# Kernel tuning notes

Measured on AMD Instinct MI355X. Metric: run time of the kernel, lower is better.

## Reference

```python
import math
import jax, jax.numpy as jnp
import numpy as np

N = 100000
E_RAND = 800000
IN_F, HID, OUT_F, HEADS = 128, 64, 64, 4
NOISE_SCALE = 1.0 * math.sqrt(2.0 * math.log(1.25 / 0.05))  # dp_rate=1, eps=1, del=0.05


def setup_inputs() -> dict:
    key = jax.random.key(0)
    ks = jax.random.split(key, 12)
    x = jax.random.normal(ks[0], (N, IN_F), dtype=jnp.float32)
    src_r = jax.random.randint(ks[1], (E_RAND,), 0, N, dtype=jnp.int32)
    dst_r = jax.random.randint(ks[2], (E_RAND,), 0, N, dtype=jnp.int32)
    loops = jnp.arange(N, dtype=jnp.int32)  # add_self_loop
    src = jnp.concatenate([src_r, loops])
    dst = jnp.concatenate([dst_r, loops])
    # layer 0: GATConv(in=128, out=64, heads=4)
    s0 = 1.0 / math.sqrt(IN_F)
    W0 = jax.random.normal(ks[3], (IN_F, HEADS * HID), dtype=jnp.float32) * s0
    al0 = jax.random.normal(ks[4], (HEADS, HID), dtype=jnp.float32) * 0.1
    ar0 = jax.random.normal(ks[5], (HEADS, HID), dtype=jnp.float32) * 0.1
    b0 = jnp.zeros((HEADS * HID,), dtype=jnp.float32)
    # layer 1: GATConv(in=256, out=64, heads=1)
    s1 = 1.0 / math.sqrt(HEADS * HID)
    W1 = jax.random.normal(ks[6], (HEADS * HID, OUT_F), dtype=jnp.float32) * s1
    al1 = jax.random.normal(ks[7], (1, OUT_F), dtype=jnp.float32) * 0.1
    ar1 = jax.random.normal(ks[8], (1, OUT_F), dtype=jnp.float32) * 0.1
    b1 = jnp.zeros((OUT_F,), dtype=jnp.float32)
    # DP gaussian noise added after first GAT layer (torch.normal(0,1,x.shape))
    noise = jax.random.normal(ks[9], (N, HEADS * HID), dtype=jnp.float32)
    return {"x": x, "src": src, "dst": dst, "W0": W0, "al0": al0, "ar0": ar0,
            "b0": b0, "W1": W1, "al1": al1, "ar1": ar1, "b1": b1, "noise": noise}


def gat_conv(x, src, dst, W, al, ar, b, apply_act):
    """DGL GATConv: per-edge attention, edge softmax over dst, scatter-sum."""
    H, D = al.shape
    h = (x @ W).reshape(-1, H, D)                      # [N,H,D]
    el = jnp.sum(h * al, axis=-1)                      # [N,H]
    er = jnp.sum(h * ar, axis=-1)                      # [N,H]
    e = jax.nn.leaky_relu(el[src] + er[dst], 0.2)      # [E,H]
    emax = jax.ops.segment_max(e, dst, num_segments=N) # [N,H]
    a = jnp.exp(e - emax[dst])
    denom = jax.ops.segment_sum(a, dst, num_segments=N)
    alpha = a / denom[dst]                             # [E,H] edge softmax
    msg = h[src] * alpha[:, :, None]                   # [E,H,D]
    out = jax.ops.segment_sum(msg, dst, num_segments=N) + b.reshape(1, H, D)
    if apply_act:
        out = jax.nn.leaky_relu(out, 0.01)             # F.leaky_relu default slope
    return out.reshape(-1, H * D)                      # flatten(1)


def reference(x, src, dst, W0, al0, ar0, b0, W1, al1, ar1, b1, noise):
    h = gat_conv(x, src, dst, W0, al0, ar0, b0, apply_act=True)   # [N, 256]
    h = h + NOISE_SCALE * noise                                   # DP noise after layer 0
    out = gat_conv(h, src, dst, W1, al1, ar1, b1, apply_act=False)  # [N, 64]
    return out
```

## Files before the change

kernel.cpp:

```cpp
#include <hip/hip_runtime.h>
#include <hip/hip_bf16.h>
#include <math.h>

#define IN_F 128
#define HID 64
#define HEADS 4
#define HD0 (HEADS * HID)
#define OUT_F 64
#define NOISE_SCALE 2.5372725354060904f

typedef __bf16 bf16x8 __attribute__((ext_vector_type(8)));
typedef float f32x4 __attribute__((ext_vector_type(4)));
typedef float f4 __attribute__((ext_vector_type(4)));
typedef unsigned int u4 __attribute__((ext_vector_type(4)));

__device__ __forceinline__ float bf2f(unsigned short u) {
    return __uint_as_float(((unsigned)u) << 16);
}
__device__ __forceinline__ unsigned short f2bf(float f) {
    unsigned u = __float_as_uint(f);
    u = u + 0x7fffu + ((u >> 16) & 1u);
    return (unsigned short)(u >> 16);
}

__device__ __forceinline__ void acc8(float* acc, const uint4& u, float wt) {
    acc[0] += wt * __uint_as_float(u.x << 16);
    acc[1] += wt * __uint_as_float(u.x & 0xffff0000u);
    acc[2] += wt * __uint_as_float(u.y << 16);
    acc[3] += wt * __uint_as_float(u.y & 0xffff0000u);
    acc[4] += wt * __uint_as_float(u.z << 16);
    acc[5] += wt * __uint_as_float(u.z & 0xffff0000u);
    acc[6] += wt * __uint_as_float(u.w << 16);
    acc[7] += wt * __uint_as_float(u.w & 0xffff0000u);
}

__device__ __forceinline__ uint4 pack8(const float4& a, const float4& b) {
    uint4 r;
    r.x = (unsigned)f2bf(a.x) | ((unsigned)f2bf(a.y) << 16);
    r.y = (unsigned)f2bf(a.z) | ((unsigned)f2bf(a.w) << 16);
    r.z = (unsigned)f2bf(b.x) | ((unsigned)f2bf(b.y) << 16);
    r.w = (unsigned)f2bf(b.z) | ((unsigned)f2bf(b.w) << 16);
    return r;
}

__global__ __launch_bounds__(256) void prep_kernel(
    int* __restrict__ deg, int N,
    unsigned long long* __restrict__ combo, int ntiles,
    const float* __restrict__ W0, unsigned short* __restrict__ W0t,
    const float* __restrict__ W1, unsigned short* __restrict__ W1t) {
    const int b = blockIdx.x;
    int i = b * 256 + threadIdx.x;
    if (i < N) deg[i] = 0;
    if (i < ntiles) combo[i] = 0ULL;
    if (b < (IN_F * HD0) / 256) {
        int n = i / IN_F, k = i % IN_F;
        W0t[i] = f2bf(W0[(size_t)k * HD0 + n]);
    } else if (b < (IN_F * HD0) / 256 + (HD0 * OUT_F) / 256) {
        int j = i - IN_F * HD0;
        int n = j / HD0, k = j % HD0;
        W1t[j] = f2bf(W1[(size_t)k * OUT_F + n]);
    }
}

template <int K, int H, int NT, bool CVT>
__global__ __launch_bounds__(256) void gemm_fused_kernel(
    const void* __restrict__ Asrc, const unsigned short* __restrict__ Bt,
    unsigned short* __restrict__ C, const float* __restrict__ al,
    const float* __restrict__ ar, float* __restrict__ el,
    float* __restrict__ er, int M, int NC) {
    constexpr int BSTR = K + 8;
    constexpr int ASTR = 40;
    constexpr int NROWS = 64 * NT;
    constexpr int CSTR = NROWS + 8;
    __shared__ __align__(16) unsigned short Bs[NROWS * BSTR];
    __shared__ __align__(16) unsigned short As[128 * ASTR];
    const unsigned short* Ab = (const unsigned short*)Asrc;
    const float* Af = (const float*)Asrc;
    const int tid = threadIdx.x;
    const int lane = tid & 63, w = tid >> 6;
    const int row0 = blockIdx.y * 128;
    const int n0 = blockIdx.x * NROWS;
    for (int i = tid; i < NROWS * (K / 8); i += 256) {
        int n = i / (K / 8), kc = i % (K / 8);
        *(uint4*)(Bs + n * BSTR + kc * 8) =
            *(const uint4*)(Bt + (size_t)(n0 + n) * K + kc * 8);
    }
    f32x4 acc[2][4 * NT] = {};
    const int q = lane >> 4, c = lane & 15;
    const int r_st = tid >> 1, hh = tid & 1;
    for (int k0 = 0; k0 < K; k0 += 32) {
        int gr = row0 + r_st;
        uint4 av0 = make_uint4(0, 0, 0, 0), av1 = make_uint4(0, 0, 0, 0);
        if (gr < M) {
            if (CVT) {
                const float* xp = Af + (size_t)gr * K + k0 + hh * 16;
                const float4 fa = *(const float4*)xp;
                const float4 fb = *(const float4*)(xp + 4);
                const float4 fc = *(const float4*)(xp + 8);
                const float4 fd = *(const float4*)(xp + 12);
                av0 = pack8(fa, fb);
                av1 = pack8(fc, fd);
            } else {
                const unsigned short* ap = Ab + (size_t)gr * K + k0 + hh * 16;
                av0 = *(const uint4*)(ap);
                av1 = *(const uint4*)(ap + 8);
            }
        }
        __syncthreads();
        *(uint4*)(As + r_st * ASTR + hh * 16) = av0;
        *(uint4*)(As + r_st * ASTR + hh * 16 + 8) = av1;
        __syncthreads();
        bf16x8 af[2], bfr[4 * NT];
        af[0] = *(const bf16x8*)(As + (w * 32 + c) * ASTR + q * 8);
        af[1] = *(const bf16x8*)(As + (w * 32 + 16 + c) * ASTR + q * 8);
#pragma unroll
        for (int nt = 0; nt < 4 * NT; ++nt)
            bfr[nt] = *(const bf16x8*)(Bs + (nt * 16 + c) * BSTR + k0 + q * 8);
#pragma unroll
        for (int mt = 0; mt < 2; ++mt)
#pragma unroll
            for (int nt = 0; nt < 4 * NT; ++nt)
                acc[mt][nt] = __builtin_amdgcn_mfma_f32_16x16x32_bf16(
                    af[mt], bfr[nt], acc[mt][nt], 0, 0, 0);
    }
    float alv[4 * NT], arv[4 * NT];
#pragma unroll
    for (int nt = 0; nt < 4 * NT; ++nt) {
        alv[nt] = al[n0 + nt * 16 + c];
        arv[nt] = ar[n0 + nt * 16 + c];
    }
    __syncthreads();
    unsigned short* Cs = Bs;
    const int headbase = n0 >> 6;
#pragma unroll
    for (int mt = 0; mt < 2; ++mt) {
#pragma unroll
        for (int r = 0; r < 4; ++r) {
            const int row = w * 32 + mt * 16 + q * 4 + r;
            const int grow = row0 + row;
            const bool ok = grow < M;
#pragma unroll
            for (int g = 0; g < NT; ++g) {
                float elp = 0.f, erp = 0.f;
#pragma unroll
                for (int t = 0; t < 4; ++t) {
                    int nt = g * 4 + t;
                    float v = acc[mt][nt][r];
                    elp += v * alv[nt];
                    erp += v * arv[nt];
                    Cs[row * CSTR + nt * 16 + c] = f2bf(v);
                }
#pragma unroll
                for (int o = 8; o > 0; o >>= 1) {
                    elp += __shfl_down(elp, o, 16);
                    erp += __shfl_down(erp, o, 16);
                }
                if (c == 0 && ok) {
                    el[(size_t)grow * H + headbase + g] = elp;
                    er[(size_t)grow * H + headbase + g] = erp;
                }
            }
        }
    }
    __syncthreads();
    constexpr int CPR = NROWS / 8;
    for (int i = tid; i < 128 * CPR; i += 256) {
        int row = i / CPR, ch = i % CPR;
        int grow = row0 + row;
        if (grow < M)
            *(uint4*)(C + (size_t)grow * NC + n0 + ch * 8) =
                *(const uint4*)(Cs + row * CSTR + ch * 8);
    }
}

__global__ __launch_bounds__(256) void degree_kernel(
    const int* __restrict__ dst, int* __restrict__ deg, int E) {
    int e = blockIdx.x * 256 + threadIdx.x;
    if (e < E) atomicAdd(&deg[dst[e]], 1);
}

__global__ __launch_bounds__(256) void scan_fused_kernel(
    const int* __restrict__ deg, int* __restrict__ off, int* __restrict__ cur,
    unsigned long long* __restrict__ combo, int N, int E) {
    const int t = blockIdx.x;
    __shared__ int s[256];
    __shared__ int sbase;
    const int tid = threadIdx.x;
    const int i = t * 256 + tid;
    const int v = (i < N) ? deg[i] : 0;
    s[tid] = v;
    __syncthreads();
    for (int d = 1; d < 256; d <<= 1) {
        int tt = (tid >= d) ? s[tid - d] : 0;
        __syncthreads();
        s[tid] += tt;
        __syncthreads();
    }
    const int tilesum = s[255];
    if (tid == 0) {
        if (t == 0) {
            atomicExch(&combo[0], (2ULL << 32) | (unsigned)tilesum);
            sbase = 0;
        } else {
            atomicExch(&combo[t], (1ULL << 32) | (unsigned)tilesum);
            int run = 0;
            int j = t - 1;
            while (true) {
                unsigned long long c;
                do {
                    c = atomicAdd(&combo[j], 0ULL);
                } while ((c >> 32) == 0ULL);
                run += (int)(c & 0xffffffffULL);
                if ((c >> 32) == 2ULL) break;
                --j;
            }
            sbase = run;
            atomicExch(&combo[t], (2ULL << 32) | (unsigned)(run + tilesum));
        }
    }
    __syncthreads();
    const int base = sbase;
    if (i < N) {
        int o = base + s[tid] - v;
        off[i] = o;
        cur[i] = o;
    }
    if (i == 0) off[N] = E;
}

__global__ __launch_bounds__(256) void fill_csr_kernel(
    const int* __restrict__ src, const int* __restrict__ dst,
    int* __restrict__ cur, int* __restrict__ csr_src, int E) {
    int e = blockIdx.x * 256 + threadIdx.x;
    if (e >= E) return;
    int d = dst[e];
    int pos = atomicAdd(&cur[d], 1);
    csr_src[pos] = src[e];
}

__global__ __launch_bounds__(256) void agg0_kernel(
    const int* __restrict__ off, const int* __restrict__ csr_src,
    const unsigned short* __restrict__ h,
    const float* __restrict__ el,
    const float* __restrict__ er,
    const float* __restrict__ b0, const float* __restrict__ noise,
    unsigned short* __restrict__ out, int N) {
    int gt = blockIdx.x * 256 + threadIdx.x;
    int n = gt >> 5;
    if (n >= N) return;
    const int lane = gt & 31;
    const int hd = lane >> 3;
    const int f0 = lane << 3;
    const float ern = er[(size_t)n * 4 + hd];
    const int beg = off[n];
    const int last = off[n + 1] - 1;
    float acc[8] = {0.f, 0.f, 0.f, 0.f, 0.f, 0.f, 0.f, 0.f};
    float l = 0.f;
    for (int p = beg; p <= last; p += 4) {
        int i1 = p + 1, i2 = p + 2, i3 = p + 3;
        const bool v1 = i1 <= last, v2 = i2 <= last, v3 = i3 <= last;
        i1 = v1 ? i1 : last;
        i2 = v2 ? i2 : last;
        i3 = v3 ? i3 : last;
        const int s0 = csr_src[p],  s1 = csr_src[i1];
        const int s2 = csr_src[i2], s3 = csr_src[i3];
        float e0 = el[(size_t)s0 * 4 + hd] + ern;
        float e1 = el[(size_t)s1 * 4 + hd] + ern;
        float e2 = el[(size_t)s2 * 4 + hd] + ern;
        float e3 = el[(size_t)s3 * 4 + hd] + ern;
        const uint4 u0 = *(const uint4*)(h + (size_t)s0 * HD0 + f0);
        const uint4 u1 = *(const uint4*)(h + (size_t)s1 * HD0 + f0);
        const uint4 u2 = *(const uint4*)(h + (size_t)s2 * HD0 + f0);
        const uint4 u3 = *(const uint4*)(h + (size_t)s3 * HD0 + f0);
        e0 = e0 > 0.f ? e0 : 0.2f * e0;
        e1 = e1 > 0.f ? e1 : 0.2f * e1;
        e2 = e2 > 0.f ? e2 : 0.2f * e2;
        e3 = e3 > 0.f ? e3 : 0.2f * e3;
        const float w0 = __expf(e0);
        const float w1 = v1 ? __expf(e1) : 0.f;
        const float w2 = v2 ? __expf(e2) : 0.f;
        const float w3 = v3 ? __expf(e3) : 0.f;
        acc8(acc, u0, w0);
        acc8(acc, u1, w1);
        acc8(acc, u2, w2);
        acc8(acc, u3, w3);
        l += (w0 + w1) + (w2 + w3);
    }
    const float rd = 1.f / l;
    const float4 ba = *(const float4*)(b0 + f0);
    const float4 bb = *(const float4*)(b0 + f0 + 4);
    const f4 na = __builtin_nontemporal_load((const f4*)(noise + (size_t)n * HD0 + f0));
    const f4 nb = __builtin_nontemporal_load((const f4*)(noise + (size_t)n * HD0 + f0 + 4));
    float o[8];
    o[0] = acc[0] * rd + ba.x;
    o[1] = acc[1] * rd + ba.y;
    o[2] = acc[2] * rd + ba.z;
    o[3] = acc[3] * rd + ba.w;
    o[4] = acc[4] * rd + bb.x;
    o[5] = acc[5] * rd + bb.y;
    o[6] = acc[6] * rd + bb.z;
    o[7] = acc[7] * rd + bb.w;
#pragma unroll
    for (int j = 0; j < 8; ++j) o[j] = o[j] > 0.f ? o[j] : 0.01f * o[j];
    o[0] += NOISE_SCALE * na.x;
    o[1] += NOISE_SCALE * na.y;
    o[2] += NOISE_SCALE * na.z;
    o[3] += NOISE_SCALE * na.w;
    o[4] += NOISE_SCALE * nb.x;
    o[5] += NOISE_SCALE * nb.y;
    o[6] += NOISE_SCALE * nb.z;
    o[7] += NOISE_SCALE * nb.w;
    uint4 ov;
    ov.x = (unsigned)f2bf(o[0]) | ((unsigned)f2bf(o[1]) << 16);
    ov.y = (unsigned)f2bf(o[2]) | ((unsigned)f2bf(o[3]) << 16);
    ov.z = (unsigned)f2bf(o[4]) | ((unsigned)f2bf(o[5]) << 16);
    ov.w = (unsigned)f2bf(o[6]) | ((unsigned)f2bf(o[7]) << 16);
    *(uint4*)(out + (size_t)n * HD0 + f0) = ov;
}

__global__ __launch_bounds__(256) void agg1_kernel(
    const int* __restrict__ off, const int* __restrict__ csr_src,
    const unsigned short* __restrict__ h,
    const float* __restrict__ el,
    const float* __restrict__ er,
    const float* __restrict__ b1, float* __restrict__ out, int N) {
    int gt = blockIdx.x * 256 + threadIdx.x;
    int n = gt >> 4;
    if (n >= N) return;
    const int lane = gt & 15;
    const int f0 = lane << 2;
    const float ern = er[n];
    const int beg = off[n];
    const int last = off[n + 1] - 1;
    float a0 = 0.f, a1 = 0.f, a2 = 0.f, a3 = 0.f, l = 0.f;
    for (int p = beg; p <= last; p += 4) {
        int i1 = p + 1, i2 = p + 2, i3 = p + 3;
        const bool v1 = i1 <= last, v2 = i2 <= last, v3 = i3 <= last;
        i1 = v1 ? i1 : last;
        i2 = v2 ? i2 : last;
        i3 = v3 ? i3 : last;
        const int s0 = csr_src[p],  s1 = csr_src[i1];
        const int s2 = csr_src[i2], s3 = csr_src[i3];
        float e0 = el[s0] + ern;
        float e1 = el[s1] + ern;
        float e2 = el[s2] + ern;
        float e3 = el[s3] + ern;
        const ushort4 u0 = *(const ushort4*)(h + (size_t)s0 * 64 + f0);
        const ushort4 u1 = *(const ushort4*)(h + (size_t)s1 * 64 + f0);
        const ushort4 u2 = *(const ushort4*)(h + (size_t)s2 * 64 + f0);
        const ushort4 u3 = *(const ushort4*)(h + (size_t)s3 * 64 + f0);
        e0 = e0 > 0.f ? e0 : 0.2f * e0;
        e1 = e1 > 0.f ? e1 : 0.2f * e1;
        e2 = e2 > 0.f ? e2 : 0.2f * e2;
        e3 = e3 > 0.f ? e3 : 0.2f * e3;
        const float w0 = __expf(e0);
        const float w1 = v1 ? __expf(e1) : 0.f;
        const float w2 = v2 ? __expf(e2) : 0.f;
        const float w3 = v3 ? __expf(e3) : 0.f;
        a0 += w0 * bf2f(u0.x) + w1 * bf2f(u1.x) + w2 * bf2f(u2.x) + w3 * bf2f(u3.x);
        a1 += w0 * bf2f(u0.y) + w1 * bf2f(u1.y) + w2 * bf2f(u2.y) + w3 * bf2f(u3.y);
        a2 += w0 * bf2f(u0.z) + w1 * bf2f(u1.z) + w2 * bf2f(u2.z) + w3 * bf2f(u3.z);
        a3 += w0 * bf2f(u0.w) + w1 * bf2f(u1.w) + w2 * bf2f(u2.w) + w3 * bf2f(u3.w);
        l += (w0 + w1) + (w2 + w3);
    }
    const float rd = 1.f / l;
    const float4 bv = *(const float4*)(b1 + f0);
    float4 o;
    o.x = a0 * rd + bv.x;
    o.y = a1 * rd + bv.y;
    o.z = a2 * rd + bv.z;
    o.w = a3 * rd + bv.w;
    *(float4*)(out + (size_t)n * 64 + f0) = o;
}

extern "C" void kernel_launch(void* const* d_in, const int* in_sizes, int n_in,
                              void* d_out, int out_size, void* d_ws, size_t ws_size,
                              hipStream_t stream) {
    const float* x     = (const float*)d_in[0];
    const int*   src   = (const int*)d_in[1];
    const int*   dst   = (const int*)d_in[2];
    const float* W0    = (const float*)d_in[3];
    const float* al0   = (const float*)d_in[4];
    const float* ar0   = (const float*)d_in[5];
    const float* b0    = (const float*)d_in[6];
    const float* W1    = (const float*)d_in[7];
    const float* al1   = (const float*)d_in[8];
    const float* ar1   = (const float*)d_in[9];
    const float* b1    = (const float*)d_in[10];
    const float* noise = (const float*)d_in[11];

    const int N = in_sizes[0] / IN_F;
    const int E = in_sizes[1];
    const int NB = (N + 255) / 256;

    char* p = (char*)d_ws;
    unsigned short* h0     = (unsigned short*)p; p += (size_t)N * HD0 * 2;
    unsigned short* agg0b  = (unsigned short*)p; p += (size_t)N * HD0 * 2;
    unsigned short* h1     = (unsigned short*)p; p += (size_t)N * OUT_F * 2;
    unsigned short* W0t    = (unsigned short*)p; p += (size_t)IN_F * HD0 * 2;
    unsigned short* W1t    = (unsigned short*)p; p += (size_t)HD0 * OUT_F * 2;
    float* el     = (float*)p; p += (size_t)N * HEADS * 4;
    float* er     = (float*)p; p += (size_t)N * HEADS * 4;
    int* deg    = (int*)p; p += (size_t)N * 4;
    int* cur    = (int*)p; p += (size_t)N * 4;
    int* off    = (int*)p; p += ((size_t)N + 4) * 4;
    unsigned long long* combo = (unsigned long long*)p; p += 512 * 8;
    int* csr_src= (int*)p; p += (size_t)E * 4;

    prep_kernel<<<NB, 256, 0, stream>>>(deg, N, combo, NB, W0, W0t, W1, W1t);

    degree_kernel<<<(E + 255) / 256, 256, 0, stream>>>(dst, deg, E);
    scan_fused_kernel<<<NB, 256, 0, stream>>>(deg, off, cur, combo, N, E);
    fill_csr_kernel<<<(E + 255) / 256, 256, 0, stream>>>(src, dst, cur, csr_src, E);

    const int MB = (N + 127) / 128;

    {
        dim3 grid(HD0 / 128, MB);
        gemm_fused_kernel<IN_F, HEADS, 2, true><<<grid, 256, 0, stream>>>(
            (const void*)x, W0t, h0, al0, ar0, el, er, N, HD0);
    }
    agg0_kernel<<<(unsigned)(((size_t)N * 32 + 255) / 256), 256, 0, stream>>>(
        off, csr_src, h0, el, er, b0, noise, agg0b, N);

    {
        dim3 grid(OUT_F / 64, MB);
        gemm_fused_kernel<HD0, 1, 1, false><<<grid, 256, 0, stream>>>(
            (const void*)agg0b, W1t, h1, al1, ar1, el, er, N, OUT_F);
    }
    agg1_kernel<<<(unsigned)(((size_t)N * 16 + 255) / 256), 256, 0, stream>>>(
        off, csr_src, h1, el, er, b1, (float*)d_out, N);
}
```

Measured before the change: 435.3 us.

## Fuse layer-1 GEMM and attention logits into layer-0 aggregation kernel

The layer-0 aggregation now stages each block's 8 output rows in shared memory as bf16 and immediately multiplies them by W1 with MFMA 16x16x32 instructions. The same kernel computes the layer-1 el/er logits through shuffle reductions and writes h1, el1 and er1 directly. This removes the 256-wide intermediate write and read and one kernel launch. In exchange, half of each 16-row MFMA tile is zero padding, a block barrier sits after the irregular gather loop, and W1 is reloaded from global memory by every block.

```diff
diff --git a/kernel.cpp b/kernel.cpp
--- a/kernel.cpp
+++ b/kernel.cpp
@@ -238,84 +238,147 @@
     csr_src[pos] = src[e];
 }
 
-__global__ __launch_bounds__(256) void agg0_kernel(
+__global__ __launch_bounds__(256) void agg0_fused_kernel(
     const int* __restrict__ off, const int* __restrict__ csr_src,
     const unsigned short* __restrict__ h,
     const float* __restrict__ el,
     const float* __restrict__ er,
     const float* __restrict__ b0, const float* __restrict__ noise,
-    unsigned short* __restrict__ out, int N) {
-    int gt = blockIdx.x * 256 + threadIdx.x;
-    int n = gt >> 5;
-    if (n >= N) return;
-    const int lane = gt & 31;
+    const unsigned short* __restrict__ W1t,
+    const float* __restrict__ al1, const float* __restrict__ ar1,
+    unsigned short* __restrict__ h1,
+    float* __restrict__ el1, float* __restrict__ er1, int N) {
+    constexpr int SSTR = 264;
+    __shared__ __align__(16) unsigned short smA[16 * SSTR];
+    __shared__ float elw[4][8], erw[4][8];
+    const int tid = threadIdx.x;
+    const int nd = tid >> 5;
+    const int n = blockIdx.x * 8 + nd;
+    const bool valid = n < N;
+    const int lane = tid & 31;
     const int hd = lane >> 3;
     const int f0 = lane << 3;
-    const float ern = er[(size_t)n * 4 + hd];
-    const int beg = off[n];
-    const int last = off[n + 1] - 1;
+    for (int i = tid; i < 264; i += 256)
+        *(uint4*)(smA + 8 * SSTR + i * 8) = make_uint4(0, 0, 0, 0);
     float acc[8] = {0.f, 0.f, 0.f, 0.f, 0.f, 0.f, 0.f, 0.f};
     float l = 0.f;
-    for (int p = beg; p <= last; p += 4) {
-        int i1 = p + 1, i2 = p + 2, i3 = p + 3;
-        const bool v1 = i1 <= last, v2 = i2 <= last, v3 = i3 <= last;
-        i1 = v1 ? i1 : last;
-        i2 = v2 ? i2 : last;
-        i3 = v3 ? i3 : last;
-        const int s0 = csr_src[p],  s1 = csr_src[i1];
-        const int s2 = csr_src[i2], s3 = csr_src[i3];
-        float e0 = el[(size_t)s0 * 4 + hd] + ern;
-        float e1 = el[(size_t)s1 * 4 + hd] + ern;
-        float e2 = el[(size_t)s2 * 4 + hd] + ern;
-        float e3 = el[(size_t)s3 * 4 + hd] + ern;
-        const uint4 u0 = *(const uint4*)(h + (size_t)s0 * HD0 + f0);
-        const uint4 u1 = *(const uint4*)(h + (size_t)s1 * HD0 + f0);
-        const uint4 u2 = *(const uint4*)(h + (size_t)s2 * HD0 + f0);
-        const uint4 u3 = *(const uint4*)(h + (size_t)s3 * HD0 + f0);
-        e0 = e0 > 0.f ? e0 : 0.2f * e0;
-        e1 = e1 > 0.f ? e1 : 0.2f * e1;
-        e2 = e2 > 0.f ? e2 : 0.2f * e2;
-        e3 = e3 > 0.f ? e3 : 0.2f * e3;
-        const float w0 = __expf(e0);
-        const float w1 = v1 ? __expf(e1) : 0.f;
-        const float w2 = v2 ? __expf(e2) : 0.f;
-        const float w3 = v3 ? __expf(e3) : 0.f;
-        acc8(acc, u0, w0);
-        acc8(acc, u1, w1);
-        acc8(acc, u2, w2);
-        acc8(acc, u3, w3);
-        l += (w0 + w1) + (w2 + w3);
-    }
-    const float rd = 1.f / l;
-    const float4 ba = *(const float4*)(b0 + f0);
-    const float4 bb = *(const float4*)(b0 + f0 + 4);
-    const f4 na = __builtin_nontemporal_load((const f4*)(noise + (size_t)n * HD0 + f0));
-    const f4 nb = __builtin_nontemporal_load((const f4*)(noise + (size_t)n * HD0 + f0 + 4));
-    float o[8];
-    o[0] = acc[0] * rd + ba.x;
-    o[1] = acc[1] * rd + ba.y;
-    o[2] = acc[2] * rd + ba.z;
-    o[3] = acc[3] * rd + ba.w;
-    o[4] = acc[4] * rd + bb.x;
-    o[5] = acc[5] * rd + bb.y;
-    o[6] = acc[6] * rd + bb.z;
-    o[7] = acc[7] * rd + bb.w;
-#pragma unroll
-    for (int j = 0; j < 8; ++j) o[j] = o[j] > 0.f ? o[j] : 0.01f * o[j];
-    o[0] += NOISE_SCALE * na.x;
-    o[1] += NOISE_SCALE * na.y;
-    o[2] += NOISE_SCALE * na.z;
-    o[3] += NOISE_SCALE * na.w;
-    o[4] += NOISE_SCALE * nb.x;
-    o[5] += NOISE_SCALE * nb.y;
-    o[6] += NOISE_SCALE * nb.z;
-    o[7] += NOISE_SCALE * nb.w;
-    uint4 ov;
-    ov.x = (unsigned)f2bf(o[0]) | ((unsigned)f2bf(o[1]) << 16);
-    ov.y = (unsigned)f2bf(o[2]) | ((unsigned)f2bf(o[3]) << 16);
-    ov.z = (unsigned)f2bf(o[4]) | ((unsigned)f2bf(o[5]) << 16);
-    ov.w = (unsigned)f2bf(o[6]) | ((unsigned)f2bf(o[7]) << 16);
-    *(uint4*)(out + (size_t)n * HD0 + f0) = ov;
+    if (valid) {
+        const float ern = er[(size_t)n * 4 + hd];
+        const int beg = off[n];
+        const int last = off[n + 1] - 1;
+        for (int p = beg; p <= last; p += 4) {
+            int i1 = p + 1, i2 = p + 2, i3 = p + 3;
+            const bool v1 = i1 <= last, v2 = i2 <= last, v3 = i3 <= last;
+            i1 = v1 ? i1 : last;
+            i2 = v2 ? i2 : last;
+            i3 = v3 ? i3 : last;
+            const int s0 = csr_src[p],  s1 = csr_src[i1];
+            const int s2 = csr_src[i2], s3 = csr_src[i3];
+            float e0 = el[(size_t)s0 * 4 + hd] + ern;
+            float e1 = el[(size_t)s1 * 4 + hd] + ern;
+            float e2 = el[(size_t)s2 * 4 + hd] + ern;
+            float e3 = el[(size_t)s3 * 4 + hd] + ern;
+            const uint4 u0 = *(const uint4*)(h + (size_t)s0 * HD0 + f0);
+            const uint4 u1 = *(const uint4*)(h + (size_t)s1 * HD0 + f0);
+            const uint4 u2 = *(const uint4*)(h + (size_t)s2 * HD0 + f0);
+            const uint4 u3 = *(const uint4*)(h + (size_t)s3 * HD0 + f0);
+            e0 = e0 > 0.f ? e0 : 0.2f * e0;
+            e1 = e1 > 0.f ? e1 : 0.2f * e1;
+            e2 = e2 > 0.f ? e2 : 0.2f * e2;
+            e3 = e3 > 0.f ? e3 : 0.2f * e3;
+            const float w0 = __expf(e0);
+            const float w1 = v1 ? __expf(e1) : 0.f;
+            const float w2 = v2 ? __expf(e2) : 0.f;
+            const float w3 = v3 ? __expf(e3) : 0.f;
+            acc8(acc, u0, w0);
+            acc8(acc, u1, w1);
+            acc8(acc, u2, w2);
+            acc8(acc, u3, w3);
+            l += (w0 + w1) + (w2 + w3);
+        }
+        const float rd = 1.f / l;
+        const float4 ba = *(const float4*)(b0 + f0);
+        const float4 bb = *(const float4*)(b0 + f0 + 4);
+        const f4 na = __builtin_nontemporal_load((const f4*)(noise + (size_t)n * HD0 + f0));
+        const f4 nb = __builtin_nontemporal_load((const f4*)(noise + (size_t)n * HD0 + f0 + 4));
+        float o[8];
+        o[0] = acc[0] * rd + ba.x;
+        o[1] = acc[1] * rd + ba.y;
+        o[2] = acc[2] * rd + ba.z;
+        o[3] = acc[3] * rd + ba.w;
+        o[4] = acc[4] * rd + bb.x;
+        o[5] = acc[5] * rd + bb.y;
+        o[6] = acc[6] * rd + bb.z;
+        o[7] = acc[7] * rd + bb.w;
+#pragma unroll
+        for (int j = 0; j < 8; ++j) o[j] = o[j] > 0.f ? o[j] : 0.01f * o[j];
+        o[0] += NOISE_SCALE * na.x;
+        o[1] += NOISE_SCALE * na.y;
+        o[2] += NOISE_SCALE * na.z;
+        o[3] += NOISE_SCALE * na.w;
+        o[4] += NOISE_SCALE * nb.x;
+        o[5] += NOISE_SCALE * nb.y;
+        o[6] += NOISE_SCALE * nb.z;
+        o[7] += NOISE_SCALE * nb.w;
+        uint4 ov;
+        ov.x = (unsigned)f2bf(o[0]) | ((unsigned)f2bf(o[1]) << 16);
+        ov.y = (unsigned)f2bf(o[2]) | ((unsigned)f2bf(o[3]) << 16);
+        ov.z = (unsigned)f2bf(o[4]) | ((unsigned)f2bf(o[5]) << 16);
+        ov.w = (unsigned)f2bf(o[6]) | ((unsigned)f2bf(o[7]) << 16);
+        *(uint4*)(smA + nd * SSTR + f0) = ov;
+    } else {
+        *(uint4*)(smA + nd * SSTR + f0) = make_uint4(0, 0, 0, 0);
+    }
+    __syncthreads();
+    const int w = tid >> 6;
+    const int q = (tid >> 4) & 3;
+    const int c = tid & 15;
+    f32x4 a2 = {};
+#pragma unroll
+    for (int k0 = 0; k0 < HD0; k0 += 32) {
+        bf16x8 af = *(const bf16x8*)(smA + c * SSTR + k0 + q * 8);
+        bf16x8 bfr = *(const bf16x8*)(W1t + (size_t)(w * 16 + c) * HD0 + k0 + q * 8);
+        a2 = __builtin_amdgcn_mfma_f32_16x16x32_bf16(af, bfr, a2, 0, 0, 0);
+    }
+    const float alv = al1[w * 16 + c];
+    const float arv = ar1[w * 16 + c];
+    float pel[4], per_[4];
+#pragma unroll
+    for (int r = 0; r < 4; ++r) {
+        pel[r] = a2[r] * alv;
+        per_[r] = a2[r] * arv;
+    }
+#pragma unroll
+    for (int m = 1; m <= 8; m <<= 1) {
+#pragma unroll
+        for (int r = 0; r < 4; ++r) {
+            pel[r] += __shfl_xor(pel[r], m);
+            per_[r] += __shfl_xor(per_[r], m);
+        }
+    }
+    if (c == 0 && q < 2) {
+#pragma unroll
+        for (int r = 0; r < 4; ++r) {
+            elw[w][q * 4 + r] = pel[r];
+            erw[w][q * 4 + r] = per_[r];
+        }
+    }
+    if (q < 2) {
+#pragma unroll
+        for (int r = 0; r < 4; ++r) {
+            int row = q * 4 + r;
+            int g = blockIdx.x * 8 + row;
+            if (g < N) h1[(size_t)g * OUT_F + w * 16 + c] = f2bf(a2[r]);
+        }
+    }
+    __syncthreads();
+    if (tid < 8) {
+        int g = blockIdx.x * 8 + tid;
+        if (g < N) {
+            el1[g] = elw[0][tid] + elw[1][tid] + elw[2][tid] + elw[3][tid];
+            er1[g] = erw[0][tid] + erw[1][tid] + erw[2][tid] + erw[3][tid];
+        }
+    }
 }
 
 __global__ __launch_bounds__(256) void agg1_kernel(
@@ -395,12 +458,13 @@
 
     char* p = (char*)d_ws;
     unsigned short* h0     = (unsigned short*)p; p += (size_t)N * HD0 * 2;
-    unsigned short* agg0b  = (unsigned short*)p; p += (size_t)N * HD0 * 2;
     unsigned short* h1     = (unsigned short*)p; p += (size_t)N * OUT_F * 2;
     unsigned short* W0t    = (unsigned short*)p; p += (size_t)IN_F * HD0 * 2;
     unsigned short* W1t    = (unsigned short*)p; p += (size_t)HD0 * OUT_F * 2;
     float* el     = (float*)p; p += (size_t)N * HEADS * 4;
     float* er     = (float*)p; p += (size_t)N * HEADS * 4;
+    float* el1    = (float*)p; p += (size_t)N * 4;
+    float* er1    = (float*)p; p += (size_t)N * 4;
     int* deg    = (int*)p; p += (size_t)N * 4;
     int* cur    = (int*)p; p += (size_t)N * 4;
     int* off    = (int*)p; p += ((size_t)N + 4) * 4;
@@ -420,14 +484,10 @@
         gemm_fused_kernel<IN_F, HEADS, 2, true><<<grid, 256, 0, stream>>>(
             (const void*)x, W0t, h0, al0, ar0, el, er, N, HD0);
     }
-    agg0_kernel<<<(unsigned)(((size_t)N * 32 + 255) / 256), 256, 0, stream>>>(
-        off, csr_src, h0, el, er, b0, noise, agg0b, N);
-
-    {
-        dim3 grid(OUT_F / 64, MB);
-        gemm_fused_kernel<HD0, 1, 1, false><<<grid, 256, 0, stream>>>(
-            (const void*)agg0b, W1t, h1, al1, ar1, el, er, N, OUT_F);
-    }
+
+    agg0_fused_kernel<<<(N + 7) / 8, 256, 0, stream>>>(
+        off, csr_src, h0, el, er, b0, noise, W1t, al1, ar1, h1, el1, er1, N);
+
     agg1_kernel<<<(unsigned)(((size_t)N * 16 + 255) / 256), 256, 0, stream>>>(
-        off, csr_src, h1, el, er, b1, (float*)d_out, N);
-}
+        off, csr_src, h1, el1, er1, b1, (float*)d_out, N);
+}
```

New measurement: 442.7 us. Within noise of the previous version (+1.7%).

## Replace layer-0 GEMM with full-width per-row-block kernel computing all heads

Applied to the files above, without the earlier changes.

Adds a dedicated layer-0 GEMM kernel in which each block converts a 128-row tile of x to bf16 once in shared memory and computes all 256 output columns. B fragments are read directly from global memory instead of being staged in LDS, and the per-head el/er dot products are computed in registers with lane shuffles. This avoids converting and loading x twice (the previous grid split the columns across two blocks) and removes the B staging step. In exchange, each thread holds a large accumulator array (32 f32x4), which may lower occupancy, and B is re-read from global/L2 by every block.

```diff
diff --git a/kernel.cpp b/kernel.cpp
--- a/kernel.cpp
+++ b/kernel.cpp
@@ -59,6 +59,91 @@
         int j = i - IN_F * HD0;
         int n = j / HD0, k = j % HD0;
         W1t[j] = f2bf(W1[(size_t)k * OUT_F + n]);
+    }
+}
+
+__global__ __launch_bounds__(256) void gemm0_kernel(
+    const float* __restrict__ x, const unsigned short* __restrict__ Bt,
+    unsigned short* __restrict__ C, const float* __restrict__ al,
+    const float* __restrict__ ar, float* __restrict__ el,
+    float* __restrict__ er, int M) {
+    constexpr int K = IN_F;
+    constexpr int ASTR = K + 8;
+    __shared__ __align__(16) unsigned short As[128 * ASTR];
+    const int tid = threadIdx.x;
+    const int lane = tid & 63, w = tid >> 6;
+    const int row0 = blockIdx.x * 128;
+    const int q = lane >> 4, c = lane & 15;
+    const int r_st = tid >> 1, hh = tid & 1;
+    {
+        const int gr = row0 + r_st;
+        const float* xp = x + (size_t)gr * K + hh * 16;
+        unsigned short* ap = As + r_st * ASTR + hh * 16;
+#pragma unroll
+        for (int k0 = 0; k0 < K; k0 += 32) {
+            uint4 av0 = make_uint4(0, 0, 0, 0), av1 = make_uint4(0, 0, 0, 0);
+            if (gr < M) {
+                const float4 fa = *(const float4*)(xp + k0);
+                const float4 fb = *(const float4*)(xp + k0 + 4);
+                const float4 fc = *(const float4*)(xp + k0 + 8);
+                const float4 fd = *(const float4*)(xp + k0 + 12);
+                av0 = pack8(fa, fb);
+                av1 = pack8(fc, fd);
+            }
+            *(uint4*)(ap + k0) = av0;
+            *(uint4*)(ap + k0 + 8) = av1;
+        }
+    }
+    __syncthreads();
+    f32x4 acc[2][16] = {};
+#pragma unroll
+    for (int k0 = 0; k0 < K; k0 += 32) {
+        const bf16x8 af0 = *(const bf16x8*)(As + (w * 32 + c) * ASTR + k0 + q * 8);
+        const bf16x8 af1 = *(const bf16x8*)(As + (w * 32 + 16 + c) * ASTR + k0 + q * 8);
+#pragma unroll
+        for (int nt = 0; nt < 16; ++nt) {
+            const bf16x8 bfr =
+                *(const bf16x8*)(Bt + (size_t)(nt * 16 + c) * K + k0 + q * 8);
+            acc[0][nt] = __builtin_amdgcn_mfma_f32_16x16x32_bf16(
+                af0, bfr, acc[0][nt], 0, 0, 0);
+            acc[1][nt] = __builtin_amdgcn_mfma_f32_16x16x32_bf16(
+                af1, bfr, acc[1][nt], 0, 0, 0);
+        }
+    }
+    float alv[16], arv[16];
+#pragma unroll
+    for (int nt = 0; nt < 16; ++nt) {
+        alv[nt] = al[nt * 16 + c];
+        arv[nt] = ar[nt * 16 + c];
+    }
+#pragma unroll
+    for (int mt = 0; mt < 2; ++mt) {
+#pragma unroll
+        for (int r = 0; r < 4; ++r) {
+            const int grow = row0 + w * 32 + mt * 16 + q * 4 + r;
+            const bool ok = grow < M;
+#pragma unroll
+            for (int g = 0; g < 4; ++g) {
+                float elp = 0.f, erp = 0.f;
+#pragma unroll
+                for (int t = 0; t < 4; ++t) {
+                    int nt = g * 4 + t;
+                    float v = acc[mt][nt][r];
+                    elp += v * alv[nt];
+                    erp += v * arv[nt];
+                    if (ok) C[(size_t)grow * HD0 + nt * 16 + c] = f2bf(v);
+                }
+#pragma unroll
+                for (int o = 8; o > 0; o >>= 1) {
+                    elp += __shfl_down(elp, o, 16);
+                    erp += __shfl_down(erp, o, 16);
+                }
+                if (c == 0 && ok) {
+                    el[(size_t)grow * HEADS + g] = elp;
+                    er[(size_t)grow * HEADS + g] = erp;
+                }
+            }
+        }
     }
 }
 
@@ -415,11 +500,8 @@
 
     const int MB = (N + 127) / 128;
 
-    {
-        dim3 grid(HD0 / 128, MB);
-        gemm_fused_kernel<IN_F, HEADS, 2, true><<<grid, 256, 0, stream>>>(
-            (const void*)x, W0t, h0, al0, ar0, el, er, N, HD0);
-    }
+    gemm0_kernel<<<MB, 256, 0, stream>>>(x, W0t, h0, al0, ar0, el, er, N);
+
     agg0_kernel<<<(unsigned)(((size_t)N * 32 + 255) / 256), 256, 0, stream>>>(
         off, csr_src, h0, el, er, b0, noise, agg0b, N);
 
@@ -428,6 +510,7 @@
         gemm_fused_kernel<HD0, 1, 1, false><<<grid, 256, 0, stream>>>(
             (const void*)agg0b, W1t, h1, al1, ar1, el, er, N, OUT_F);
     }
+
     agg1_kernel<<<(unsigned)(((size_t)N * 16 + 255) / 256), 256, 0, stream>>>(
         off, csr_src, h1, el, er, b1, (float*)d_out, N);
 }
```

Measured after the change: 475.8 us. 1.09x slower.
